# Optimization experiments

Measured on AMD Instinct MI355X. Metric: run time of the kernel, lower is better.

The kernel has to match this reference:

```python
import jax, jax.numpy as jnp
import numpy as np

NEG_INF = -9.0e15  # matches torch's -9000000000000000.0 mask value
ALPHA = 0.2        # LeakyReLU negative slope from init_kwargs


def setup_inputs() -> dict:
    key = jax.random.key(0)
    k1, k2, k3, k4, k5 = jax.random.split(key, 5)
    B, N, D, A = 64, 128, 128, 1000
    hidden = jax.random.normal(k1, (B, N, D), dtype=jnp.float32)
    adj = jax.random.randint(k2, (B, N, N), 0, 5)  # edge types 0..4 (0 = masked)
    a = jax.random.normal(k3, (D, 4), dtype=jnp.float32) * 0.1  # stacked a_0..a_3
    A_attr_sess = jax.random.uniform(k4, (B, N, A), dtype=jnp.float32)
    attr_embedding = jax.random.normal(k5, (A, D), dtype=jnp.float32)
    return {"hidden": hidden, "adj": adj, "a": a,
            "A_attr_sess": A_attr_sess, "attr_embedding": attr_embedding}


def reference(hidden, adj, a, A_attr_sess, attr_embedding):
    # a_input[b,i,j,:] = leaky_relu(h[b,i,:] * h[b,j,:])  -> [B,N,N,D]
    a_input = jax.nn.leaky_relu(hidden[:, :, None, :] * hidden[:, None, :, :],
                                negative_slope=ALPHA)
    # four edge-type scores in one contraction: [B,N,N,4]
    e = jnp.einsum('bijd,dk->bijk', a_input, a)
    # masked selection by adjacency edge type (later writes override earlier)
    alpha = jnp.full(adj.shape, NEG_INF, dtype=e.dtype)
    alpha = jnp.where(adj == 1, e[..., 0], alpha)
    alpha = jnp.where(adj == 2, e[..., 1], alpha)
    alpha = jnp.where(adj == 3, e[..., 2], alpha)
    alpha = jnp.where(adj == 4, e[..., 3], alpha)
    attn = jax.nn.softmax(alpha, axis=-1)        # [B,N,N]
    output = jnp.einsum('bij,bjd->bid', attn, hidden)  # [B,N,D]
    attr_sess = jnp.einsum('bna,ad->bnd', A_attr_sess, attr_embedding)
    return output, attr_sess
```

## Files before the change

kernel.cpp:

```cpp
#include <hip/hip_runtime.h>

#define BB 64
#define NN 128
#define DD 128
#define AA 1000
#define KPAD 1024
#define NEG_INF (-9.0e15f)

typedef __attribute__((ext_vector_type(8))) short short8;
typedef __attribute__((ext_vector_type(4))) float floatx4;
typedef __attribute__((ext_vector_type(4))) unsigned int uintx4;

__device__ __forceinline__ float bflo(unsigned int u) { return __uint_as_float(u << 16); }
__device__ __forceinline__ float bfhi(unsigned int u) { return __uint_as_float(u & 0xffff0000u); }
__device__ __forceinline__ unsigned int packbf(float f0, float f1) {
  return (__float_as_uint(f0) >> 16) | (__float_as_uint(f1) & 0xffff0000u);
}
__device__ __forceinline__ unsigned short bf_rne(float f) {
  unsigned int u = __float_as_uint(f);
  return (unsigned short)((u + 0x7fffu + ((u >> 16) & 1u)) >> 16);
}
__device__ __forceinline__ unsigned int packbf_rne(float f0, float f1) {
  return (unsigned int)bf_rne(f0) | ((unsigned int)bf_rne(f1) << 16);
}
__device__ __forceinline__ short8 u2s(uintx4 v) {
  union { uintx4 u; short8 s; } x; x.u = v; return x.s;
}
__device__ __forceinline__ float rne_f(float x, unsigned int msk) {
  return __uint_as_float(((unsigned int)bf_rne(x) & msk) << 16);
}

__global__ __launch_bounds__(256) void prep_kernel(
    const float* __restrict__ hidden, const float* __restrict__ emb,
    const float* __restrict__ amat,
    unsigned short* __restrict__ ET, unsigned short* __restrict__ HTg,
    unsigned short* __restrict__ Hg, unsigned short* __restrict__ Asg)
{
  __shared__ float hsf[NN * 129];
  __shared__ float safk[256];
  const int t = threadIdx.x;
  const int bid = blockIdx.x;
  if (bid < BB) {
    const float* hb = hidden + (size_t)bid * NN * DD;
    #pragma unroll
    for (int u = 0; u < 16; ++u) {
      int e = u * 1024 + t * 4;
      float4 v = *reinterpret_cast<const float4*>(hb + e);
      int r = e >> 7, c = e & 127;
      float* d = &hsf[r * 129 + c];
      d[0] = v.x; d[1] = v.y; d[2] = v.z; d[3] = v.w;
    }
    __syncthreads();
    unsigned short* ht16 = HTg + (size_t)bid * NN * DD;
    #pragma unroll
    for (int u = 0; u < 8; ++u) {
      int e = u * 2048 + t * 8;
      int dI = e >> 7, il = e & 127;
      float x[8];
      #pragma unroll
      for (int j = 0; j < 8; ++j) x[j] = hsf[(il + j) * 129 + dI];
      uintx4 o;
      o.x = packbf_rne(x[0], x[1]); o.y = packbf_rne(x[2], x[3]);
      o.z = packbf_rne(x[4], x[5]); o.w = packbf_rne(x[6], x[7]);
      *reinterpret_cast<uintx4*>(ht16 + e) = o;
    }
    unsigned short* hg = Hg + (size_t)bid * NN * DD;
    #pragma unroll
    for (int u = 0; u < 8; ++u) {
      int id = u * 256 + t;
      int r = id >> 4, c = id & 15;
      const float* src = &hsf[r * 129 + c * 8];
      uintx4 o;
      o.x = packbf_rne(src[0], src[1]); o.y = packbf_rne(src[2], src[3]);
      o.z = packbf_rne(src[4], src[5]); o.w = packbf_rne(src[6], src[7]);
      *reinterpret_cast<uintx4*>(hg + r * 128 + c * 8) = o;
    }
  } else if (bid < BB + 32) {
    const int k0 = (bid - BB) * 32;
    #pragma unroll
    for (int u = 0; u < 4; ++u) {
      int e = u * 1024 + t * 4;
      int r = e >> 7, c = e & 127;
      float4 z = {0.f, 0.f, 0.f, 0.f};
      float4 v = (k0 + r < AA)
          ? *reinterpret_cast<const float4*>(emb + (size_t)(k0 + r) * DD + c) : z;
      float* d = &hsf[r * 129 + c];
      d[0] = v.x; d[1] = v.y; d[2] = v.z; d[3] = v.w;
    }
    __syncthreads();
    int c = t >> 1, j0 = (t & 1) * 16;
    float x[16];
    #pragma unroll
    for (int j = 0; j < 16; ++j) x[j] = hsf[(j0 + j) * 129 + c];
    uintx4 o0, o1;
    o0.x = packbf_rne(x[0], x[1]);  o0.y = packbf_rne(x[2], x[3]);
    o0.z = packbf_rne(x[4], x[5]);  o0.w = packbf_rne(x[6], x[7]);
    o1.x = packbf_rne(x[8], x[9]);  o1.y = packbf_rne(x[10], x[11]);
    o1.z = packbf_rne(x[12], x[13]); o1.w = packbf_rne(x[14], x[15]);
    unsigned short* dst = ET + (size_t)c * KPAD + k0 + j0;
    *reinterpret_cast<uintx4*>(dst) = o0;
    *reinterpret_cast<uintx4*>(dst + 8) = o1;
  } else {
    const int idx = bid - BB - 32;
    const int b = idx >> 2, k = idx & 3;
    safk[t] = ((t & 128) ? 0.4f : 0.6f) * amat[(t & 127) * 4 + k];
    __syncthreads();
    const float* hb = hidden + (size_t)b * NN * DD;
    unsigned short* ag = Asg + ((size_t)b * NN * 4 + k) * 256;
    #pragma unroll
    for (int u = 0; u < 16; ++u) {
      int id = u * 256 + t;
      int i = id >> 5, c = id & 31;
      const float* src = hb + i * DD + (c & 15) * 8;
      float4 v0 = *reinterpret_cast<const float4*>(src);
      float4 v1 = *reinterpret_cast<const float4*>(src + 4);
      unsigned int msk = (c & 16) ? 0x7fffu : 0xffffu;
      float ve0 = rne_f(v0.x, msk), ve1 = rne_f(v0.y, msk);
      float ve2 = rne_f(v0.z, msk), ve3 = rne_f(v0.w, msk);
      float ve4 = rne_f(v1.x, msk), ve5 = rne_f(v1.y, msk);
      float ve6 = rne_f(v1.z, msk), ve7 = rne_f(v1.w, msk);
      const float* sf = &safk[c * 8];
      uintx4 o;
      o.x = packbf(ve0 * sf[0], ve1 * sf[1]);
      o.y = packbf(ve2 * sf[2], ve3 * sf[3]);
      o.z = packbf(ve4 * sf[4], ve5 * sf[5]);
      o.w = packbf(ve6 * sf[6], ve7 * sf[7]);
      *reinterpret_cast<uintx4*>(ag + (size_t)i * 1024 + c * 8) = o;
    }
  }
}

struct FS {
  __align__(16) float Sa[16 * 129];
  __align__(16) unsigned short W[16 * 128];
};

__global__ __launch_bounds__(256, 4) void fused_kernel(
    const int* __restrict__ adj, const float* __restrict__ Aattr,
    const unsigned short* __restrict__ ET, const unsigned short* __restrict__ HTg,
    const unsigned short* __restrict__ Hg, const unsigned short* __restrict__ Asg,
    float* __restrict__ out0, float* __restrict__ out1)
{
  __shared__ FS s;
  const int t = threadIdx.x;
  const int L = t & 63, w = t >> 6;
  const int lr = L & 15, lq = L >> 4;
  const int bid = blockIdx.x;
  const int wid = (bid & 7) * 128 + (bid >> 3);
  const int tile = wid >> 1;

  if ((wid & 1) == 0) {
    const int b = tile >> 3;
    const int i0 = (tile & 7) * 16;

    const int* adjb = adj + ((size_t)b * NN + i0) * NN;
    int adjv[8];
    #pragma unroll
    for (int nt = 0; nt < 2; ++nt)
      #pragma unroll
      for (int r = 0; r < 4; ++r)
        adjv[nt * 4 + r] = adjb[(lq * 4 + r) * NN + w * 32 + nt * 16 + lr];

    const unsigned short* hg = Hg + (size_t)b * NN * DD;
    uintx4 hvq[2][4];
    #pragma unroll
    for (int nt = 0; nt < 2; ++nt)
      #pragma unroll
      for (int q = 0; q < 4; ++q) {
        int jrow = w * 32 + nt * 16 + lr;
        hvq[nt][q] = *reinterpret_cast<const uintx4*>(
            hg + jrow * 128 + (lq + 4 * q) * 8);
      }

    const unsigned short* ag = Asg + ((size_t)(b * NN + i0 + lr)) * 4 * 256;
    floatx4 acc[4][2];
    #pragma unroll
    for (int k = 0; k < 4; ++k)
      #pragma unroll
      for (int nt = 0; nt < 2; ++nt) acc[k][nt] = floatx4{0.f, 0.f, 0.f, 0.f};

    #pragma unroll
    for (int kt = 0; kt < 8; ++kt) {
      int ca = lq + 4 * kt;
      short8 afr[4];
      #pragma unroll
      for (int k = 0; k < 4; ++k)
        afr[k] = *reinterpret_cast<const short8*>(ag + k * 256 + ca * 8);
      #pragma unroll
      for (int nt = 0; nt < 2; ++nt) {
        uintx4 hv = hvq[nt][kt & 3];
        if (kt >= 4) {
          hv.x &= 0x7fff7fffu; hv.y &= 0x7fff7fffu;
          hv.z &= 0x7fff7fffu; hv.w &= 0x7fff7fffu;
        }
        short8 bfr = u2s(hv);
        #pragma unroll
        for (int k = 0; k < 4; ++k)
          acc[k][nt] = __builtin_amdgcn_mfma_f32_16x16x32_bf16(
              afr[k], bfr, acc[k][nt], 0, 0, 0);
      }
    }

    short8 pvb[2][4];
    const unsigned short* ht = HTg + (size_t)b * NN * DD;
    #pragma unroll
    for (int nt = 0; nt < 2; ++nt)
      #pragma unroll
      for (int kt = 0; kt < 4; ++kt) {
        int dI = w * 32 + nt * 16 + lr;
        pvb[nt][kt] = *reinterpret_cast<const short8*>(
            ht + dI * 128 + kt * 32 + lq * 8);
      }

    #pragma unroll
    for (int nt = 0; nt < 2; ++nt)
      #pragma unroll
      for (int r = 0; r < 4; ++r) {
        int ii = lq * 4 + r;
        int j = w * 32 + nt * 16 + lr;
        int ad = adjv[nt * 4 + r];
        float al = NEG_INF;
        al = (ad == 1) ? acc[0][nt][r] : al;
        al = (ad == 2) ? acc[1][nt][r] : al;
        al = (ad == 3) ? acc[2][nt][r] : al;
        al = (ad == 4) ? acc[3][nt][r] : al;
        s.Sa[ii * 129 + j] = al;
      }
    __syncthreads();

    #pragma unroll
    for (int p = 0; p < 4; ++p) {
      int ii = w * 4 + p;
      float a1 = s.Sa[ii * 129 + L];
      float a2 = s.Sa[ii * 129 + 64 + L];
      float m = fmaxf(a1, a2);
      #pragma unroll
      for (int off = 32; off > 0; off >>= 1) m = fmaxf(m, __shfl_xor(m, off, 64));
      float e1 = __expf(fmaxf(a1 - m, -80.f));
      float e2 = __expf(fmaxf(a2 - m, -80.f));
      float ss = e1 + e2;
      #pragma unroll
      for (int off = 32; off > 0; off >>= 1) ss += __shfl_xor(ss, off, 64);
      float inv = 1.f / ss;
      int j2 = L + 64;
      s.W[ii * 128 + (((L >> 3) ^ ii) << 3) + (L & 7)] = bf_rne(e1 * inv);
      s.W[ii * 128 + (((j2 >> 3) ^ ii) << 3) + (j2 & 7)] = bf_rne(e2 * inv);
    }
    __syncthreads();

    floatx4 oacc0 = floatx4{0.f, 0.f, 0.f, 0.f};
    floatx4 oacc1 = floatx4{0.f, 0.f, 0.f, 0.f};
    #pragma unroll
    for (int kt = 0; kt < 4; ++kt) {
      int c = lq + 4 * kt;
      short8 wf = *reinterpret_cast<const short8*>(
          &s.W[lr * 128 + ((c ^ lr) << 3)]);
      oacc0 = __builtin_amdgcn_mfma_f32_16x16x32_bf16(wf, pvb[0][kt], oacc0, 0, 0, 0);
      oacc1 = __builtin_amdgcn_mfma_f32_16x16x32_bf16(wf, pvb[1][kt], oacc1, 0, 0, 0);
    }
    float* ob = out0 + ((size_t)b * NN + i0) * DD;
    #pragma unroll
    for (int r = 0; r < 4; ++r) {
      ob[(lq * 4 + r) * DD + w * 32 + lr] = oacc0[r];
      ob[(lq * 4 + r) * DD + w * 32 + 16 + lr] = oacc1[r];
    }
  } else {
    const int r0 = tile * 16;
    const float* arow = Aattr + (size_t)(r0 + lr) * AA;
    const unsigned short* e0 = ET + (size_t)(w * 32 + lr) * KPAD;
    const unsigned short* e1 = ET + (size_t)(w * 32 + 16 + lr) * KPAD;

    float4 paA[4], paB[4];
    uintx4 peA[4], peB[4];
    floatx4 acc0 = floatx4{0.f, 0.f, 0.f, 0.f};
    floatx4 acc1 = floatx4{0.f, 0.f, 0.f, 0.f};

#define AFETCH(PA, PE, IT) do {                                              \
    int kb = (IT) * 64;                                                      \
    float4 z = {0.f, 0.f, 0.f, 0.f};                                        \
    _Pragma("unroll")                                                        \
    for (int ks = 0; ks < 2; ++ks) {                                         \
      int k4 = kb + (lq + 4 * ks) * 8;                                       \
      PA[ks * 2 + 0] = (k4 < AA) ? *reinterpret_cast<const float4*>(arow + k4) : z; \
      PA[ks * 2 + 1] = (k4 + 4 < AA) ? *reinterpret_cast<const float4*>(arow + k4 + 4) : z; \
      PE[ks * 2 + 0] = *reinterpret_cast<const uintx4*>(e0 + k4);            \
      PE[ks * 2 + 1] = *reinterpret_cast<const uintx4*>(e1 + k4);            \
    }                                                                        \
  } while (0)

#define ABODY(PA, PE, IT) do {                                               \
    short8 af0, af1, bf00, bf01, bf10, bf11;                                 \
    {                                                                        \
      uintx4 a0, a1;                                                         \
      a0.x = packbf(PA[0].x, PA[0].y); a0.y = packbf(PA[0].z, PA[0].w);      \
      a0.z = packbf(PA[1].x, PA[1].y); a0.w = packbf(PA[1].z, PA[1].w);      \
      a1.x = packbf(PA[2].x, PA[2].y); a1.y = packbf(PA[2].z, PA[2].w);      \
      a1.z = packbf(PA[3].x, PA[3].y); a1.w = packbf(PA[3].z, PA[3].w);      \
      af0 = u2s(a0); af1 = u2s(a1);                                          \
      bf00 = u2s(PE[0]); bf01 = u2s(PE[1]);                                  \
      bf10 = u2s(PE[2]); bf11 = u2s(PE[3]);                                  \
    }                                                                        \
    if ((IT) < 14) AFETCH(PA, PE, (IT) + 2);                                 \
    acc0 = __builtin_amdgcn_mfma_f32_16x16x32_bf16(af0, bf00, acc0, 0, 0, 0); \
    acc1 = __builtin_amdgcn_mfma_f32_16x16x32_bf16(af0, bf01, acc1, 0, 0, 0); \
    acc0 = __builtin_amdgcn_mfma_f32_16x16x32_bf16(af1, bf10, acc0, 0, 0, 0); \
    acc1 = __builtin_amdgcn_mfma_f32_16x16x32_bf16(af1, bf11, acc1, 0, 0, 0); \
  } while (0)

    AFETCH(paA, peA, 0);
    AFETCH(paB, peB, 1);
    #pragma unroll
    for (int ith = 0; ith < 8; ++ith) {
      ABODY(paA, peA, 2 * ith);
      ABODY(paB, peB, 2 * ith + 1);
    }
#undef AFETCH
#undef ABODY

    float* ob = out1 + (size_t)r0 * DD;
    #pragma unroll
    for (int r = 0; r < 4; ++r) {
      ob[(lq * 4 + r) * DD + w * 32 + lr] = acc0[r];
      ob[(lq * 4 + r) * DD + w * 32 + 16 + lr] = acc1[r];
    }
  }
}

extern "C" void kernel_launch(void* const* d_in, const int* in_sizes, int n_in,
                              void* d_out, int out_size, void* d_ws, size_t ws_size,
                              hipStream_t stream) {
  const float* hidden = (const float*)d_in[0];
  const int*   adj    = (const int*)d_in[1];
  const float* amat   = (const float*)d_in[2];
  const float* Aattr  = (const float*)d_in[3];
  const float* emb    = (const float*)d_in[4];

  float* out0 = (float*)d_out;
  float* out1 = out0 + (size_t)BB * NN * DD;

  unsigned short* ET  = (unsigned short*)d_ws;
  unsigned short* HTg = ET + (size_t)DD * KPAD;
  unsigned short* Hg  = HTg + (size_t)BB * NN * DD;
  unsigned short* Asg = Hg + (size_t)BB * NN * DD;

  prep_kernel<<<BB + 32 + 256, 256, 0, stream>>>(hidden, emb, amat,
                                                 ET, HTg, Hg, Asg);
  fused_kernel<<<1024, 256, 0, stream>>>(adj, Aattr, ET, HTg, Hg, Asg,
                                         out0, out1);
}
```

Baseline: 130.1 us.

## Split fused kernel into attention and attribute kernels with swizzled LDS-staged A tiles

Replaces the single interleaved fused kernel with two kernels: one for graph attention and one for the attribute matmul. The prep kernel now writes the scaled A operand in a per-tile, XOR-swizzled layout. The attention kernel loads that tile cooperatively into LDS so the MFMA A fragments come from shared memory instead of strided global reads. The attribute kernel deepens its register prefetch from two to three stages. The cost is an extra kernel launch, the loss of overlap between the two workloads, and lower occupancy from launch_bounds(256,2) plus the larger LDS union.

Result: faster. 125.0 us (-3.9%).

```diff
diff --git a/kernel.cpp b/kernel.cpp
--- a/kernel.cpp
+++ b/kernel.cpp
@@ -37,7 +37,7 @@
     unsigned short* __restrict__ Hg, unsigned short* __restrict__ Asg)
 {
   __shared__ float hsf[NN * 129];
-  __shared__ float safk[256];
+  __shared__ float safk[1024];
   const int t = threadIdx.x;
   const int bid = blockIdx.x;
   if (bid < BB) {
@@ -102,16 +102,21 @@
     *reinterpret_cast<uintx4*>(dst + 8) = o1;
   } else {
     const int idx = bid - BB - 32;
-    const int b = idx >> 2, k = idx & 3;
-    safk[t] = ((t & 128) ? 0.4f : 0.6f) * amat[(t & 127) * 4 + k];
+    const int b = idx >> 2, iq = idx & 3;
+    #pragma unroll
+    for (int q = 0; q < 4; ++q) {
+      int idq = q * 256 + t;
+      int k = idq >> 8, dp = idq & 255;
+      safk[idq] = ((dp & 128) ? 0.4f : 0.6f) * amat[(dp & 127) * 4 + k];
+    }
     __syncthreads();
-    const float* hb = hidden + (size_t)b * NN * DD;
-    unsigned short* ag = Asg + ((size_t)b * NN * 4 + k) * 256;
-    #pragma unroll
-    for (int u = 0; u < 16; ++u) {
-      int id = u * 256 + t;
-      int i = id >> 5, c = id & 31;
-      const float* src = hb + i * DD + (c & 15) * 8;
+    const float* hb = hidden + ((size_t)b * NN + iq * 32) * DD;
+    unsigned short* ag = Asg + ((size_t)b * 8 + iq * 2) * 16384;
+    #pragma unroll
+    for (int v = 0; v < 16; ++v) {
+      int id = v * 256 + t;
+      int il = id >> 7, k = (id >> 5) & 3, c = id & 31;
+      const float* src = hb + il * DD + (c & 15) * 8;
       float4 v0 = *reinterpret_cast<const float4*>(src);
       float4 v1 = *reinterpret_cast<const float4*>(src + 4);
       unsigned int msk = (c & 16) ? 0x7fffu : 0xffffu;
@@ -119,161 +124,180 @@
       float ve2 = rne_f(v0.z, msk), ve3 = rne_f(v0.w, msk);
       float ve4 = rne_f(v1.x, msk), ve5 = rne_f(v1.y, msk);
       float ve6 = rne_f(v1.z, msk), ve7 = rne_f(v1.w, msk);
-      const float* sf = &safk[c * 8];
+      const float* sf = &safk[k * 256 + c * 8];
       uintx4 o;
       o.x = packbf(ve0 * sf[0], ve1 * sf[1]);
       o.y = packbf(ve2 * sf[2], ve3 * sf[3]);
       o.z = packbf(ve4 * sf[4], ve5 * sf[5]);
       o.w = packbf(ve6 * sf[6], ve7 * sf[7]);
-      *reinterpret_cast<uintx4*>(ag + (size_t)i * 1024 + c * 8) = o;
-    }
-  }
-}
-
-struct FS {
-  __align__(16) float Sa[16 * 129];
-  __align__(16) unsigned short W[16 * 128];
-};
-
-__global__ __launch_bounds__(256, 4) void fused_kernel(
-    const int* __restrict__ adj, const float* __restrict__ Aattr,
-    const unsigned short* __restrict__ ET, const unsigned short* __restrict__ HTg,
-    const unsigned short* __restrict__ Hg, const unsigned short* __restrict__ Asg,
-    float* __restrict__ out0, float* __restrict__ out1)
+      *reinterpret_cast<uintx4*>(
+          ag + (il >> 4) * 16384 + k * 4096 + (il & 15) * 256
+             + ((c ^ (il & 15)) << 3)) = o;
+    }
+  }
+}
+
+__global__ __launch_bounds__(256, 2) void attn_kernel(
+    const int* __restrict__ adj,
+    const unsigned short* __restrict__ HTg, const unsigned short* __restrict__ Hg,
+    const unsigned short* __restrict__ Asg, float* __restrict__ out0)
 {
-  __shared__ FS s;
+  __shared__ union {
+    unsigned short As[4 * 16 * 256];
+    struct { float Sa[16 * 129]; unsigned short W[16 * 128]; } sw;
+  } uu;
   const int t = threadIdx.x;
   const int L = t & 63, w = t >> 6;
   const int lr = L & 15, lq = L >> 4;
   const int bid = blockIdx.x;
-  const int wid = (bid & 7) * 128 + (bid >> 3);
-  const int tile = wid >> 1;
-
-  if ((wid & 1) == 0) {
-    const int b = tile >> 3;
-    const int i0 = (tile & 7) * 16;
-
-    const int* adjb = adj + ((size_t)b * NN + i0) * NN;
-    int adjv[8];
-    #pragma unroll
-    for (int nt = 0; nt < 2; ++nt)
-      #pragma unroll
-      for (int r = 0; r < 4; ++r)
-        adjv[nt * 4 + r] = adjb[(lq * 4 + r) * NN + w * 32 + nt * 16 + lr];
-
-    const unsigned short* hg = Hg + (size_t)b * NN * DD;
-    uintx4 hvq[2][4];
-    #pragma unroll
-    for (int nt = 0; nt < 2; ++nt)
-      #pragma unroll
-      for (int q = 0; q < 4; ++q) {
-        int jrow = w * 32 + nt * 16 + lr;
-        hvq[nt][q] = *reinterpret_cast<const uintx4*>(
-            hg + jrow * 128 + (lq + 4 * q) * 8);
+  const int wid = (bid & 7) * 64 + (bid >> 3);
+  const int b = wid >> 3;
+  const int i0 = (wid & 7) * 16;
+
+  const unsigned short* ags = Asg + (size_t)wid * 16384;
+  uintx4 asv[8];
+  #pragma unroll
+  for (int u = 0; u < 8; ++u)
+    asv[u] = *reinterpret_cast<const uintx4*>(ags + (u * 256 + t) * 8);
+
+  const int* adjb = adj + ((size_t)b * NN + i0) * NN;
+  int adjv[8];
+  #pragma unroll
+  for (int nt = 0; nt < 2; ++nt)
+    #pragma unroll
+    for (int r = 0; r < 4; ++r)
+      adjv[nt * 4 + r] = adjb[(lq * 4 + r) * NN + w * 32 + nt * 16 + lr];
+
+  const unsigned short* hg = Hg + (size_t)b * NN * DD;
+  uintx4 hvq[2][4];
+  #pragma unroll
+  for (int nt = 0; nt < 2; ++nt)
+    #pragma unroll
+    for (int q = 0; q < 4; ++q) {
+      int jrow = w * 32 + nt * 16 + lr;
+      hvq[nt][q] = *reinterpret_cast<const uintx4*>(
+          hg + jrow * 128 + (lq + 4 * q) * 8);
+    }
+
+  short8 pvb[2][4];
+  const unsigned short* ht = HTg + (size_t)b * NN * DD;
+  #pragma unroll
+  for (int nt = 0; nt < 2; ++nt)
+    #pragma unroll
+    for (int kt = 0; kt < 4; ++kt) {
+      int dI = w * 32 + nt * 16 + lr;
+      pvb[nt][kt] = *reinterpret_cast<const short8*>(
+          ht + dI * 128 + kt * 32 + lq * 8);
+    }
+
+  #pragma unroll
+  for (int u = 0; u < 8; ++u)
+    *reinterpret_cast<uintx4*>(&uu.As[(u * 256 + t) * 8]) = asv[u];
+  __syncthreads();
+
+  floatx4 acc[4][2];
+  #pragma unroll
+  for (int k = 0; k < 4; ++k)
+    #pragma unroll
+    for (int nt = 0; nt < 2; ++nt) acc[k][nt] = floatx4{0.f, 0.f, 0.f, 0.f};
+
+  #pragma unroll
+  for (int kt = 0; kt < 8; ++kt) {
+    int ca = lq + 4 * kt;
+    short8 afr[4];
+    #pragma unroll
+    for (int k = 0; k < 4; ++k)
+      afr[k] = *reinterpret_cast<const short8*>(
+          &uu.As[k * 4096 + lr * 256 + ((ca ^ lr) << 3)]);
+    #pragma unroll
+    for (int nt = 0; nt < 2; ++nt) {
+      uintx4 hv = hvq[nt][kt & 3];
+      if (kt >= 4) {
+        hv.x &= 0x7fff7fffu; hv.y &= 0x7fff7fffu;
+        hv.z &= 0x7fff7fffu; hv.w &= 0x7fff7fffu;
       }
-
-    const unsigned short* ag = Asg + ((size_t)(b * NN + i0 + lr)) * 4 * 256;
-    floatx4 acc[4][2];
-    #pragma unroll
-    for (int k = 0; k < 4; ++k)
-      #pragma unroll
-      for (int nt = 0; nt < 2; ++nt) acc[k][nt] = floatx4{0.f, 0.f, 0.f, 0.f};
-
-    #pragma unroll
-    for (int kt = 0; kt < 8; ++kt) {
-      int ca = lq + 4 * kt;
-      short8 afr[4];
+      short8 bfr = u2s(hv);
       #pragma unroll
       for (int k = 0; k < 4; ++k)
-        afr[k] = *reinterpret_cast<const short8*>(ag + k * 256 + ca * 8);
-      #pragma unroll
-      for (int nt = 0; nt < 2; ++nt) {
-        uintx4 hv = hvq[nt][kt & 3];
-        if (kt >= 4) {
-          hv.x &= 0x7fff7fffu; hv.y &= 0x7fff7fffu;
-          hv.z &= 0x7fff7fffu; hv.w &= 0x7fff7fffu;
-        }
-        short8 bfr = u2s(hv);
-        #pragma unroll
-        for (int k = 0; k < 4; ++k)
-          acc[k][nt] = __builtin_amdgcn_mfma_f32_16x16x32_bf16(
-              afr[k], bfr, acc[k][nt], 0, 0, 0);
-      }
-    }
-
-    short8 pvb[2][4];
-    const unsigned short* ht = HTg + (size_t)b * NN * DD;
-    #pragma unroll
-    for (int nt = 0; nt < 2; ++nt)
-      #pragma unroll
-      for (int kt = 0; kt < 4; ++kt) {
-        int dI = w * 32 + nt * 16 + lr;
-        pvb[nt][kt] = *reinterpret_cast<const short8*>(
-            ht + dI * 128 + kt * 32 + lq * 8);
-      }
-
-    #pragma unroll
-    for (int nt = 0; nt < 2; ++nt)
-      #pragma unroll
-      for (int r = 0; r < 4; ++r) {
-        int ii = lq * 4 + r;
-        int j = w * 32 + nt * 16 + lr;
-        int ad = adjv[nt * 4 + r];
-        float al = NEG_INF;
-        al = (ad == 1) ? acc[0][nt][r] : al;
-        al = (ad == 2) ? acc[1][nt][r] : al;
-        al = (ad == 3) ? acc[2][nt][r] : al;
-        al = (ad == 4) ? acc[3][nt][r] : al;
-        s.Sa[ii * 129 + j] = al;
-      }
-    __syncthreads();
-
-    #pragma unroll
-    for (int p = 0; p < 4; ++p) {
-      int ii = w * 4 + p;
-      float a1 = s.Sa[ii * 129 + L];
-      float a2 = s.Sa[ii * 129 + 64 + L];
-      float m = fmaxf(a1, a2);
-      #pragma unroll
-      for (int off = 32; off > 0; off >>= 1) m = fmaxf(m, __shfl_xor(m, off, 64));
-      float e1 = __expf(fmaxf(a1 - m, -80.f));
-      float e2 = __expf(fmaxf(a2 - m, -80.f));
-      float ss = e1 + e2;
-      #pragma unroll
-      for (int off = 32; off > 0; off >>= 1) ss += __shfl_xor(ss, off, 64);
-      float inv = 1.f / ss;
-      int j2 = L + 64;
-      s.W[ii * 128 + (((L >> 3) ^ ii) << 3) + (L & 7)] = bf_rne(e1 * inv);
-      s.W[ii * 128 + (((j2 >> 3) ^ ii) << 3) + (j2 & 7)] = bf_rne(e2 * inv);
-    }
-    __syncthreads();
-
-    floatx4 oacc0 = floatx4{0.f, 0.f, 0.f, 0.f};
-    floatx4 oacc1 = floatx4{0.f, 0.f, 0.f, 0.f};
-    #pragma unroll
-    for (int kt = 0; kt < 4; ++kt) {
-      int c = lq + 4 * kt;
-      short8 wf = *reinterpret_cast<const short8*>(
-          &s.W[lr * 128 + ((c ^ lr) << 3)]);
-      oacc0 = __builtin_amdgcn_mfma_f32_16x16x32_bf16(wf, pvb[0][kt], oacc0, 0, 0, 0);
-      oacc1 = __builtin_amdgcn_mfma_f32_16x16x32_bf16(wf, pvb[1][kt], oacc1, 0, 0, 0);
-    }
-    float* ob = out0 + ((size_t)b * NN + i0) * DD;
+        acc[k][nt] = __builtin_amdgcn_mfma_f32_16x16x32_bf16(
+            afr[k], bfr, acc[k][nt], 0, 0, 0);
+    }
+  }
+  __syncthreads();
+
+  #pragma unroll
+  for (int nt = 0; nt < 2; ++nt)
     #pragma unroll
     for (int r = 0; r < 4; ++r) {
-      ob[(lq * 4 + r) * DD + w * 32 + lr] = oacc0[r];
-      ob[(lq * 4 + r) * DD + w * 32 + 16 + lr] = oacc1[r];
-    }
-  } else {
-    const int r0 = tile * 16;
-    const float* arow = Aattr + (size_t)(r0 + lr) * AA;
-    const unsigned short* e0 = ET + (size_t)(w * 32 + lr) * KPAD;
-    const unsigned short* e1 = ET + (size_t)(w * 32 + 16 + lr) * KPAD;
-
-    float4 paA[4], paB[4];
-    uintx4 peA[4], peB[4];
-    floatx4 acc0 = floatx4{0.f, 0.f, 0.f, 0.f};
-    floatx4 acc1 = floatx4{0.f, 0.f, 0.f, 0.f};
+      int ii = lq * 4 + r;
+      int j = w * 32 + nt * 16 + lr;
+      int ad = adjv[nt * 4 + r];
+      float al = NEG_INF;
+      al = (ad == 1) ? acc[0][nt][r] : al;
+      al = (ad == 2) ? acc[1][nt][r] : al;
+      al = (ad == 3) ? acc[2][nt][r] : al;
+      al = (ad == 4) ? acc[3][nt][r] : al;
+      uu.sw.Sa[ii * 129 + j] = al;
+    }
+  __syncthreads();
+
+  #pragma unroll
+  for (int p = 0; p < 4; ++p) {
+    int ii = w * 4 + p;
+    float a1 = uu.sw.Sa[ii * 129 + L];
+    float a2 = uu.sw.Sa[ii * 129 + 64 + L];
+    float m = fmaxf(a1, a2);
+    #pragma unroll
+    for (int off = 32; off > 0; off >>= 1) m = fmaxf(m, __shfl_xor(m, off, 64));
+    float e1 = __expf(fmaxf(a1 - m, -80.f));
+    float e2 = __expf(fmaxf(a2 - m, -80.f));
+    float ss = e1 + e2;
+    #pragma unroll
+    for (int off = 32; off > 0; off >>= 1) ss += __shfl_xor(ss, off, 64);
+    float inv = 1.f / ss;
+    int j2 = L + 64;
+    uu.sw.W[ii * 128 + (((L >> 3) ^ ii) << 3) + (L & 7)] = bf_rne(e1 * inv);
+    uu.sw.W[ii * 128 + (((j2 >> 3) ^ ii) << 3) + (j2 & 7)] = bf_rne(e2 * inv);
+  }
+  __syncthreads();
+
+  floatx4 oacc0 = floatx4{0.f, 0.f, 0.f, 0.f};
+  floatx4 oacc1 = floatx4{0.f, 0.f, 0.f, 0.f};
+  #pragma unroll
+  for (int kt = 0; kt < 4; ++kt) {
+    int c = lq + 4 * kt;
+    short8 wf = *reinterpret_cast<const short8*>(
+        &uu.sw.W[lr * 128 + ((c ^ lr) << 3)]);
+    oacc0 = __builtin_amdgcn_mfma_f32_16x16x32_bf16(wf, pvb[0][kt], oacc0, 0, 0, 0);
+    oacc1 = __builtin_amdgcn_mfma_f32_16x16x32_bf16(wf, pvb[1][kt], oacc1, 0, 0, 0);
+  }
+  float* ob = out0 + ((size_t)b * NN + i0) * DD;
+  #pragma unroll
+  for (int r = 0; r < 4; ++r) {
+    ob[(lq * 4 + r) * DD + w * 32 + lr] = oacc0[r];
+    ob[(lq * 4 + r) * DD + w * 32 + 16 + lr] = oacc1[r];
+  }
+}
+
+__global__ __launch_bounds__(256, 2) void attr_kernel(
+    const float* __restrict__ Aattr, const unsigned short* __restrict__ ET,
+    float* __restrict__ out1)
+{
+  const int t = threadIdx.x;
+  const int L = t & 63, w = t >> 6;
+  const int lr = L & 15, lq = L >> 4;
+  const int bid = blockIdx.x;
+  const int wid = (bid & 7) * 64 + (bid >> 3);
+  const int r0 = wid * 16;
+
+  const float* arow = Aattr + (size_t)(r0 + lr) * AA;
+  const unsigned short* e0 = ET + (size_t)(w * 32 + lr) * KPAD;
+  const unsigned short* e1 = ET + (size_t)(w * 32 + 16 + lr) * KPAD;
+
+  float4 paA[4], paB[4], paC[4];
+  uintx4 peA[4], peB[4], peC[4];
+  floatx4 acc0 = floatx4{0.f, 0.f, 0.f, 0.f};
+  floatx4 acc1 = floatx4{0.f, 0.f, 0.f, 0.f};
 
 #define AFETCH(PA, PE, IT) do {                                              \
     int kb = (IT) * 64;                                                      \
@@ -300,29 +324,30 @@
       bf00 = u2s(PE[0]); bf01 = u2s(PE[1]);                                  \
       bf10 = u2s(PE[2]); bf11 = u2s(PE[3]);                                  \
     }                                                                        \
-    if ((IT) < 14) AFETCH(PA, PE, (IT) + 2);                                 \
+    if ((IT) < 13) AFETCH(PA, PE, (IT) + 3);                                 \
     acc0 = __builtin_amdgcn_mfma_f32_16x16x32_bf16(af0, bf00, acc0, 0, 0, 0); \
     acc1 = __builtin_amdgcn_mfma_f32_16x16x32_bf16(af0, bf01, acc1, 0, 0, 0); \
     acc0 = __builtin_amdgcn_mfma_f32_16x16x32_bf16(af1, bf10, acc0, 0, 0, 0); \
     acc1 = __builtin_amdgcn_mfma_f32_16x16x32_bf16(af1, bf11, acc1, 0, 0, 0); \
   } while (0)
 
-    AFETCH(paA, peA, 0);
-    AFETCH(paB, peB, 1);
-    #pragma unroll
-    for (int ith = 0; ith < 8; ++ith) {
-      ABODY(paA, peA, 2 * ith);
-      ABODY(paB, peB, 2 * ith + 1);
-    }
+  AFETCH(paA, peA, 0);
+  AFETCH(paB, peB, 1);
+  AFETCH(paC, peC, 2);
+  ABODY(paA, peA, 0);  ABODY(paB, peB, 1);  ABODY(paC, peC, 2);
+  ABODY(paA, peA, 3);  ABODY(paB, peB, 4);  ABODY(paC, peC, 5);
+  ABODY(paA, peA, 6);  ABODY(paB, peB, 7);  ABODY(paC, peC, 8);
+  ABODY(paA, peA, 9);  ABODY(paB, peB, 10); ABODY(paC, peC, 11);
+  ABODY(paA, peA, 12); ABODY(paB, peB, 13); ABODY(paC, peC, 14);
+  ABODY(paA, peA, 15);
 #undef AFETCH
 #undef ABODY
 
-    float* ob = out1 + (size_t)r0 * DD;
-    #pragma unroll
-    for (int r = 0; r < 4; ++r) {
-      ob[(lq * 4 + r) * DD + w * 32 + lr] = acc0[r];
-      ob[(lq * 4 + r) * DD + w * 32 + 16 + lr] = acc1[r];
-    }
+  float* ob = out1 + (size_t)r0 * DD;
+  #pragma unroll
+  for (int r = 0; r < 4; ++r) {
+    ob[(lq * 4 + r) * DD + w * 32 + lr] = acc0[r];
+    ob[(lq * 4 + r) * DD + w * 32 + 16 + lr] = acc1[r];
   }
 }
 
@@ -345,6 +370,6 @@
 
   prep_kernel<<<BB + 32 + 256, 256, 0, stream>>>(hidden, emb, amat,
                                                  ET, HTg, Hg, Asg);
-  fused_kernel<<<1024, 256, 0, stream>>>(adj, Aattr, ET, HTg, Hg, Asg,
-                                         out0, out1);
-}
+  attn_kernel<<<512, 256, 0, stream>>>(adj, HTg, Hg, Asg, out0);
+  attr_kernel<<<512, 256, 0, stream>>>(Aattr, ET, out1);
+}
```

## Build scaled attention A-operands in shared memory inside fused kernel

Applied to the files above, without the earlier changes.

Stops precomputing the per-row, per-edge-type scaled bf16 A operands (Asg) in the prep kernel and writing them to global memory. The fused kernel now loads the bf16 hidden rows, scales them by the a-vector coefficients, and stores them into swizzled LDS, unioned with the softmax scratch buffers. This removes 256 prep blocks and a sizable global write and read round trip. In exchange it adds LDS usage, extra barriers and on-the-fly scaling work in each attention block, which may reduce occupancy.

After: 124.0 us. -4.7%, faster.

```diff
diff --git a/kernel.cpp b/kernel.cpp
--- a/kernel.cpp
+++ b/kernel.cpp
@@ -26,18 +26,13 @@
 __device__ __forceinline__ short8 u2s(uintx4 v) {
   union { uintx4 u; short8 s; } x; x.u = v; return x.s;
 }
-__device__ __forceinline__ float rne_f(float x, unsigned int msk) {
-  return __uint_as_float(((unsigned int)bf_rne(x) & msk) << 16);
-}
 
 __global__ __launch_bounds__(256) void prep_kernel(
     const float* __restrict__ hidden, const float* __restrict__ emb,
-    const float* __restrict__ amat,
     unsigned short* __restrict__ ET, unsigned short* __restrict__ HTg,
-    unsigned short* __restrict__ Hg, unsigned short* __restrict__ Asg)
+    unsigned short* __restrict__ Hg)
 {
   __shared__ float hsf[NN * 129];
-  __shared__ float safk[256];
   const int t = threadIdx.x;
   const int bid = blockIdx.x;
   if (bid < BB) {
@@ -75,7 +70,7 @@
       o.z = packbf_rne(src[4], src[5]); o.w = packbf_rne(src[6], src[7]);
       *reinterpret_cast<uintx4*>(hg + r * 128 + c * 8) = o;
     }
-  } else if (bid < BB + 32) {
+  } else {
     const int k0 = (bid - BB) * 32;
     #pragma unroll
     for (int u = 0; u < 4; ++u) {
@@ -100,48 +95,27 @@
     unsigned short* dst = ET + (size_t)c * KPAD + k0 + j0;
     *reinterpret_cast<uintx4*>(dst) = o0;
     *reinterpret_cast<uintx4*>(dst + 8) = o1;
-  } else {
-    const int idx = bid - BB - 32;
-    const int b = idx >> 2, k = idx & 3;
-    safk[t] = ((t & 128) ? 0.4f : 0.6f) * amat[(t & 127) * 4 + k];
-    __syncthreads();
-    const float* hb = hidden + (size_t)b * NN * DD;
-    unsigned short* ag = Asg + ((size_t)b * NN * 4 + k) * 256;
-    #pragma unroll
-    for (int u = 0; u < 16; ++u) {
-      int id = u * 256 + t;
-      int i = id >> 5, c = id & 31;
-      const float* src = hb + i * DD + (c & 15) * 8;
-      float4 v0 = *reinterpret_cast<const float4*>(src);
-      float4 v1 = *reinterpret_cast<const float4*>(src + 4);
-      unsigned int msk = (c & 16) ? 0x7fffu : 0xffffu;
-      float ve0 = rne_f(v0.x, msk), ve1 = rne_f(v0.y, msk);
-      float ve2 = rne_f(v0.z, msk), ve3 = rne_f(v0.w, msk);
-      float ve4 = rne_f(v1.x, msk), ve5 = rne_f(v1.y, msk);
-      float ve6 = rne_f(v1.z, msk), ve7 = rne_f(v1.w, msk);
-      const float* sf = &safk[c * 8];
-      uintx4 o;
-      o.x = packbf(ve0 * sf[0], ve1 * sf[1]);
-      o.y = packbf(ve2 * sf[2], ve3 * sf[3]);
-      o.z = packbf(ve4 * sf[4], ve5 * sf[5]);
-      o.w = packbf(ve6 * sf[6], ve7 * sf[7]);
-      *reinterpret_cast<uintx4*>(ag + (size_t)i * 1024 + c * 8) = o;
-    }
   }
 }
 
-struct FS {
-  __align__(16) float Sa[16 * 129];
-  __align__(16) unsigned short W[16 * 128];
+struct AttnSmem {
+  union {
+    __align__(16) unsigned short As[4 * 16 * 256];
+    struct {
+      __align__(16) float Sa[16 * 129];
+      __align__(16) unsigned short W[16 * 128];
+    } sw;
+  } u2;
+  __align__(16) float saf[4 * 256];
 };
 
 __global__ __launch_bounds__(256, 4) void fused_kernel(
-    const int* __restrict__ adj, const float* __restrict__ Aattr,
-    const unsigned short* __restrict__ ET, const unsigned short* __restrict__ HTg,
-    const unsigned short* __restrict__ Hg, const unsigned short* __restrict__ Asg,
+    const int* __restrict__ adj, const float* __restrict__ amat,
+    const float* __restrict__ Aattr, const unsigned short* __restrict__ ET,
+    const unsigned short* __restrict__ HTg, const unsigned short* __restrict__ Hg,
     float* __restrict__ out0, float* __restrict__ out1)
 {
-  __shared__ FS s;
+  __shared__ AttnSmem s;
   const int t = threadIdx.x;
   const int L = t & 63, w = t >> 6;
   const int lr = L & 15, lq = L >> 4;
@@ -152,7 +126,16 @@
   if ((wid & 1) == 0) {
     const int b = tile >> 3;
     const int i0 = (tile & 7) * 16;
-
+    const unsigned short* hg = Hg + (size_t)b * NN * DD;
+
+    uintx4 asrc[8];
+    #pragma unroll
+    for (int u = 0; u < 8; ++u) {
+      int id = u * 256 + t;
+      int ii = (id >> 5) & 15, c = id & 31;
+      asrc[u] = *reinterpret_cast<const uintx4*>(
+          hg + (i0 + ii) * 128 + (c & 15) * 8);
+    }
     const int* adjb = adj + ((size_t)b * NN + i0) * NN;
     int adjv[8];
     #pragma unroll
@@ -160,8 +143,6 @@
       #pragma unroll
       for (int r = 0; r < 4; ++r)
         adjv[nt * 4 + r] = adjb[(lq * 4 + r) * NN + w * 32 + nt * 16 + lr];
-
-    const unsigned short* hg = Hg + (size_t)b * NN * DD;
     uintx4 hvq[2][4];
     #pragma unroll
     for (int nt = 0; nt < 2; ++nt)
@@ -171,8 +152,35 @@
         hvq[nt][q] = *reinterpret_cast<const uintx4*>(
             hg + jrow * 128 + (lq + 4 * q) * 8);
       }
-
-    const unsigned short* ag = Asg + ((size_t)(b * NN + i0 + lr)) * 4 * 256;
+    {
+      float v1 = amat[t], v2 = amat[t + 256];
+      int dI = t >> 2, k = t & 3;
+      s.saf[k * 256 + dI] = 0.6f * v1;
+      s.saf[k * 256 + 128 + dI] = 0.4f * v1;
+      s.saf[k * 256 + 64 + dI] = 0.6f * v2;
+      s.saf[k * 256 + 192 + dI] = 0.4f * v2;
+    }
+    __syncthreads();
+
+    #pragma unroll
+    for (int u = 0; u < 8; ++u) {
+      int id = u * 256 + t;
+      int k = id >> 9, ii = (id >> 5) & 15, c = id & 31;
+      uintx4 hv = asrc[u];
+      if (c & 16) {
+        hv.x &= 0x7fff7fffu; hv.y &= 0x7fff7fffu;
+        hv.z &= 0x7fff7fffu; hv.w &= 0x7fff7fffu;
+      }
+      const float* sf = &s.saf[k * 256 + c * 8];
+      uintx4 o;
+      o.x = packbf(bflo(hv.x) * sf[0], bfhi(hv.x) * sf[1]);
+      o.y = packbf(bflo(hv.y) * sf[2], bfhi(hv.y) * sf[3]);
+      o.z = packbf(bflo(hv.z) * sf[4], bfhi(hv.z) * sf[5]);
+      o.w = packbf(bflo(hv.w) * sf[6], bfhi(hv.w) * sf[7]);
+      *reinterpret_cast<uintx4*>(&s.u2.As[k * 4096 + ii * 256 + ((c ^ ii) << 3)]) = o;
+    }
+    __syncthreads();
+
     floatx4 acc[4][2];
     #pragma unroll
     for (int k = 0; k < 4; ++k)
@@ -185,7 +193,8 @@
       short8 afr[4];
       #pragma unroll
       for (int k = 0; k < 4; ++k)
-        afr[k] = *reinterpret_cast<const short8*>(ag + k * 256 + ca * 8);
+        afr[k] = *reinterpret_cast<const short8*>(
+            &s.u2.As[k * 4096 + lr * 256 + ((ca ^ lr) << 3)]);
       #pragma unroll
       for (int nt = 0; nt < 2; ++nt) {
         uintx4 hv = hvq[nt][kt & 3];
@@ -200,6 +209,7 @@
               afr[k], bfr, acc[k][nt], 0, 0, 0);
       }
     }
+    __syncthreads();
 
     short8 pvb[2][4];
     const unsigned short* ht = HTg + (size_t)b * NN * DD;
@@ -224,15 +234,15 @@
         al = (ad == 2) ? acc[1][nt][r] : al;
         al = (ad == 3) ? acc[2][nt][r] : al;
         al = (ad == 4) ? acc[3][nt][r] : al;
-        s.Sa[ii * 129 + j] = al;
+        s.u2.sw.Sa[ii * 129 + j] = al;
       }
     __syncthreads();
 
     #pragma unroll
     for (int p = 0; p < 4; ++p) {
       int ii = w * 4 + p;
-      float a1 = s.Sa[ii * 129 + L];
-      float a2 = s.Sa[ii * 129 + 64 + L];
+      float a1 = s.u2.sw.Sa[ii * 129 + L];
+      float a2 = s.u2.sw.Sa[ii * 129 + 64 + L];
       float m = fmaxf(a1, a2);
       #pragma unroll
       for (int off = 32; off > 0; off >>= 1) m = fmaxf(m, __shfl_xor(m, off, 64));
@@ -243,8 +253,8 @@
       for (int off = 32; off > 0; off >>= 1) ss += __shfl_xor(ss, off, 64);
       float inv = 1.f / ss;
       int j2 = L + 64;
-      s.W[ii * 128 + (((L >> 3) ^ ii) << 3) + (L & 7)] = bf_rne(e1 * inv);
-      s.W[ii * 128 + (((j2 >> 3) ^ ii) << 3) + (j2 & 7)] = bf_rne(e2 * inv);
+      s.u2.sw.W[ii * 128 + (((L >> 3) ^ ii) << 3) + (L & 7)] = bf_rne(e1 * inv);
+      s.u2.sw.W[ii * 128 + (((j2 >> 3) ^ ii) << 3) + (j2 & 7)] = bf_rne(e2 * inv);
     }
     __syncthreads();
 
@@ -254,7 +264,7 @@
     for (int kt = 0; kt < 4; ++kt) {
       int c = lq + 4 * kt;
       short8 wf = *reinterpret_cast<const short8*>(
-          &s.W[lr * 128 + ((c ^ lr) << 3)]);
+          &s.u2.sw.W[lr * 128 + ((c ^ lr) << 3)]);
       oacc0 = __builtin_amdgcn_mfma_f32_16x16x32_bf16(wf, pvb[0][kt], oacc0, 0, 0, 0);
       oacc1 = __builtin_amdgcn_mfma_f32_16x16x32_bf16(wf, pvb[1][kt], oacc1, 0, 0, 0);
     }
@@ -341,10 +351,8 @@
   unsigned short* ET  = (unsigned short*)d_ws;
   unsigned short* HTg = ET + (size_t)DD * KPAD;
   unsigned short* Hg  = HTg + (size_t)BB * NN * DD;
-  unsigned short* Asg = Hg + (size_t)BB * NN * DD;
-
-  prep_kernel<<<BB + 32 + 256, 256, 0, stream>>>(hidden, emb, amat,
-                                                 ET, HTg, Hg, Asg);
-  fused_kernel<<<1024, 256, 0, stream>>>(adj, Aattr, ET, HTg, Hg, Asg,
+
+  prep_kernel<<<BB + 32, 256, 0, stream>>>(hidden, emb, ET, HTg, Hg);
+  fused_kernel<<<1024, 256, 0, stream>>>(adj, amat, Aattr, ET, HTg, Hg,
                                          out0, out1);
 }
```
